# Performance work log

Hardware: AMD Instinct MI355X
Metric: run time of the kernel (lower is better)

The kernel has to match this reference:

```python
import jax, jax.numpy as jnp
import numpy as np

N_QUBITS = 9
N_CIR = 8
CHUNK = 256  # 2**(N_QUBITS-1)
DIM = 512    # 2**N_QUBITS

# Fixed gate sequence (kind, param_index, wires) transcribed from the qnode.
GATES = []
GATES += [("ry", i, (i,)) for i in range(9)]
GATES += [("rx", 9 + i, (i,)) for i in range(9)]
GATES += [("xx", 18 + k, w) for k, w in enumerate([(0,1),(8,7),(1,2),(7,6),(2,3),(6,5),(3,4),(5,4)])]
GATES += [("cry", 26 + k, w) for k, w in enumerate([(0,1),(1,2),(2,3),(8,7),(7,6),(6,5),(5,4),(3,4)])]
GATES += [("ry", 34 + i, (i,)) for i in range(9)]
GATES += [("xy", 43 + k, w) for k, w in enumerate([(4,3),(4,5),(3,2),(5,6),(2,1),(6,7),(1,0),(7,8)])]
GATES += [("crx", 51 + k, w) for k, w in enumerate([(0,1),(2,3),(5,6),(7,8),(1,2),(6,7)])]
GATES += [("rx", 57 + i, (i,)) for i in range(9)]
GATES += [("xx", 66 + k, w) for k, w in enumerate([(0,1),(8,7),(1,2),(7,6),(2,3),(6,5),(3,4),(5,4)])]
GATES += [("cry", 74 + k, w) for k, w in enumerate([(0,1),(1,2),(2,3),(8,7),(7,6),(6,5),(5,4),(3,4)])]
GATES += [("ry", 82 + i, (i,)) for i in range(9)]
GATES += [("xy", 91 + k, w) for k, w in enumerate([(4,3),(4,5),(3,2),(5,6),(2,1),(6,7),(1,0),(7,8)])]
GATES += [("crx", 99 + k, w) for k, w in enumerate([(0,1),(2,3),(5,6),(7,8),(1,2),(6,7)])]
GATES += [("rx", 105 + i, (i,)) for i in range(9)]
assert len(GATES) == 114

C64 = jnp.complex64

def _ry(t):
    c = jnp.cos(t / 2).astype(C64); s = jnp.sin(t / 2).astype(C64)
    return jnp.stack([jnp.stack([c, -s]), jnp.stack([s, c])])

def _rx(t):
    c = jnp.cos(t / 2).astype(C64); s = (-1j * jnp.sin(t / 2)).astype(C64)
    return jnp.stack([jnp.stack([c, s]), jnp.stack([s, c])])

def _xx(t):  # exp(-i t/2 XX)
    c = jnp.cos(t / 2).astype(C64); s = (-1j * jnp.sin(t / 2)).astype(C64)
    z = jnp.zeros_like(c)
    return jnp.stack([jnp.stack([c, z, z, s]), jnp.stack([z, c, s, z]),
                      jnp.stack([z, s, c, z]), jnp.stack([s, z, z, c])])

def _xy(t):  # PennyLane IsingXY
    c = jnp.cos(t / 2).astype(C64); s = (1j * jnp.sin(t / 2)).astype(C64)
    o = jnp.ones_like(c); z = jnp.zeros_like(c)
    return jnp.stack([jnp.stack([o, z, z, z]), jnp.stack([z, c, s, z]),
                      jnp.stack([z, s, c, z]), jnp.stack([z, z, z, o])])

def _ctrl(u2):  # block-diag(I2, u2): control on wires[0], target wires[1]
    z2 = jnp.zeros((2, 2), u2.dtype); i2 = jnp.eye(2, dtype=u2.dtype)
    return jnp.concatenate([jnp.concatenate([i2, z2], 1), jnp.concatenate([z2, u2], 1)], 0)

def _apply1(st, u, w):
    ax = 1 + w
    t = jnp.moveaxis(st, ax, -1)
    t = jnp.einsum('...a,ba->...b', t, u)
    return jnp.moveaxis(t, -1, ax)

def _apply2(st, u, w0, w1):
    a0, a1 = 1 + w0, 1 + w1
    t = jnp.moveaxis(st, (a0, a1), (-2, -1))
    sh = t.shape
    t = jnp.einsum('...a,ba->...b', t.reshape(sh[:-2] + (4,)), u).reshape(sh)
    return jnp.moveaxis(t, (-2, -1), (a0, a1))

def _circuit_probs(feats, qw):
    # feats: (N, 256) float32 -> analytic probs (N, 512)
    f = feats / jnp.linalg.norm(feats, axis=-1, keepdims=True)
    N = f.shape[0]
    # AmplitudeEmbedding on wires [0,1,2,3,5,6,7,8]; wire 4 stays |0>.
    st = jnp.stack([f.reshape(N, 16, 16), jnp.zeros((N, 16, 16), f.dtype)], axis=2)
    st = st.reshape((N,) + (2,) * N_QUBITS).astype(C64)
    for kind, idx, w in GATES:
        t = qw[idx]
        if kind == 'ry':
            st = _apply1(st, _ry(t), w[0])
        elif kind == 'rx':
            st = _apply1(st, _rx(t), w[0])
        elif kind == 'xx':
            st = _apply2(st, _xx(t), *w)
        elif kind == 'xy':
            st = _apply2(st, _xy(t), *w)
        elif kind == 'cry':
            st = _apply2(st, _ctrl(_ry(t)), *w)
        else:  # crx
            st = _apply2(st, _ctrl(_rx(t)), *w)
    return (st.real ** 2 + st.imag ** 2).reshape(N, DIM).astype(jnp.float32)


def setup_inputs() -> dict:
    key = jax.random.key(0)
    k1, k2 = jax.random.split(key)
    B = 4096
    return {
        "input_features": jax.random.normal(k1, (B, N_CIR * CHUNK), dtype=jnp.float32),
        "q_params": jax.random.normal(k2, (114,), dtype=jnp.float32),  # q_delta=1
    }


def reference(input_features, q_params):
    B = input_features.shape[0]
    q_in = jnp.tanh(input_features) * (np.pi / 2.0)
    chunks = q_in.reshape(B * N_CIR, CHUNK)          # per-sample split into 8 chunks of 256
    probs = _circuit_probs(chunks, q_params)          # (B*8, 512), all circuits batched
    return probs.reshape(B, 1024, 2, 2)
```

## Files before the change

kernel.cpp:

```cpp
#include <hip/hip_runtime.h>
#include <utility>

typedef __attribute__((ext_vector_type(8))) short short8;
typedef __attribute__((ext_vector_type(4))) float f32x4;
typedef unsigned short u16;

#define NROW 32768
#define KDIM 256
#define NOUT 512

static constexpr unsigned char cGK[114] = {
  0,0,0,0,0,0,0,0,0,
  1,1,1,1,1,1,1,1,1,
  2,2,2,2,2,2,2,2,
  4,4,4,4,4,4,4,4,
  0,0,0,0,0,0,0,0,0,
  3,3,3,3,3,3,3,3,
  5,5,5,5,5,5,
  1,1,1,1,1,1,1,1,1,
  2,2,2,2,2,2,2,2,
  4,4,4,4,4,4,4,4,
  0,0,0,0,0,0,0,0,0,
  3,3,3,3,3,3,3,3,
  5,5,5,5,5,5,
  1,1,1,1,1,1,1,1,1
};
static constexpr unsigned char cGW0[114] = {
  0,1,2,3,4,5,6,7,8,
  0,1,2,3,4,5,6,7,8,
  0,8,1,7,2,6,3,5,
  0,1,2,8,7,6,5,3,
  0,1,2,3,4,5,6,7,8,
  4,4,3,5,2,6,1,7,
  0,2,5,7,1,6,
  0,1,2,3,4,5,6,7,8,
  0,8,1,7,2,6,3,5,
  0,1,2,8,7,6,5,3,
  0,1,2,3,4,5,6,7,8,
  4,4,3,5,2,6,1,7,
  0,2,5,7,1,6,
  0,1,2,3,4,5,6,7,8
};
static constexpr unsigned char cGW1[114] = {
  0,0,0,0,0,0,0,0,0,
  0,0,0,0,0,0,0,0,0,
  1,7,2,6,3,5,4,4,
  1,2,3,7,6,5,4,4,
  0,0,0,0,0,0,0,0,0,
  3,5,2,6,1,7,0,8,
  1,3,6,8,2,7,
  0,0,0,0,0,0,0,0,0,
  1,7,2,6,3,5,4,4,
  1,2,3,7,6,5,4,4,
  0,0,0,0,0,0,0,0,0,
  3,5,2,6,1,7,0,8,
  1,3,6,8,2,7,
  0,0,0,0,0,0,0,0,0
};

__device__ __forceinline__ u16 f2bf(float f) {
  unsigned int u = __float_as_uint(f);
  u = (u + 0x7fffu + ((u >> 16) & 1u)) >> 16;
  return (u16)u;
}
__device__ __forceinline__ float bf2f(u16 b) {
  return __uint_as_float(((unsigned int)b) << 16);
}

__device__ __forceinline__ float fast_tanh(float x) {
  float xc = fminf(x, 15.f);
  float e = __expf(2.f * xc);
  return 1.f - 2.f * __builtin_amdgcn_rcpf(e + 1.f);
}

typedef const __attribute__((address_space(1))) unsigned int* gptr_t;
typedef __attribute__((address_space(3))) unsigned int* lptr_t;
__device__ __forceinline__ void gload16(const void* g, void* l) {
  __builtin_amdgcn_global_load_lds((gptr_t)g, (lptr_t)l, 16, 0, 0);
}

template <int G>
__device__ __forceinline__ void apply_gate(float (&re)[8], float (&im)[8],
                                           float c0v, float s0v, float c1v,
                                           float s1v, int l) {
  constexpr int kind = cGK[G];
  constexpr int p0 = 8 - cGW0[G];
  constexpr int p1 = 8 - cGW1[G];
  constexpr int m = (kind <= 1) ? (1 << p0)
                  : (kind <= 3) ? ((1 << p0) | (1 << p1))
                  : (1 << p1);
  constexpr int ml = m & 63;
  constexpr int mr = m >> 6;
  float c = __shfl((G < 64) ? c0v : c1v, G & 63, 64);
  float s = __shfl((G < 64) ? s0v : s1v, G & 63, 64);
  float br[8], bi[8];
  #pragma unroll
  for (int r = 0; r < 8; ++r) { br[r] = re[r ^ mr]; bi[r] = im[r ^ mr]; }
  if constexpr (ml != 0) {
    #pragma unroll
    for (int r = 0; r < 8; ++r) {
      br[r] = __shfl_xor(br[r], ml, 64);
      bi[r] = __shfl_xor(bi[r], ml, 64);
    }
  }
  #pragma unroll
  for (int r = 0; r < 8; ++r) {
    const int idx = (r << 6) | l;
    float nre, nim;
    if constexpr (kind == 0) {
      float sg = ((idx >> p0) & 1) ? s : -s;
      nre = c * re[r] + sg * br[r];
      nim = c * im[r] + sg * bi[r];
    } else if constexpr (kind == 1 || kind == 2) {
      nre = c * re[r] + s * bi[r];
      nim = c * im[r] - s * br[r];
    } else if constexpr (kind == 3) {
      bool ap = (((idx >> p0) ^ (idx >> p1)) & 1) != 0;
      nre = ap ? (c * re[r] - s * bi[r]) : re[r];
      nim = ap ? (c * im[r] + s * br[r]) : im[r];
    } else if constexpr (kind == 4) {
      bool ap = ((idx >> p0) & 1) != 0;
      float sg = ((idx >> p1) & 1) ? s : -s;
      nre = ap ? (c * re[r] + sg * br[r]) : re[r];
      nim = ap ? (c * im[r] + sg * bi[r]) : im[r];
    } else {
      bool ap = ((idx >> p0) & 1) != 0;
      nre = ap ? (c * re[r] + s * bi[r]) : re[r];
      nim = ap ? (c * im[r] - s * br[r]) : im[r];
    }
    re[r] = nre; im[r] = nim;
  }
}

template <int... Gs>
__device__ __forceinline__ void apply_all(std::integer_sequence<int, Gs...>,
                                          float (&re)[8], float (&im)[8],
                                          float c0v, float s0v, float c1v,
                                          float s1v, int l) {
  (apply_gate<Gs>(re, im, c0v, s0v, c1v, s1v, l), ...);
}

__global__ void __launch_bounds__(256) prep_build(
    const float* __restrict__ x, const float* __restrict__ qp,
    u16* __restrict__ G, float* __restrict__ invn2, u16* __restrict__ BreT,
    u16* __restrict__ BimT) {
  int bid = blockIdx.x;
  int tid = threadIdx.x;
  int l = tid & 63;
  if (bid < 64) {
    int k = bid * 4 + (tid >> 6);
    float a0 = qp[l] * 0.5f;
    float a1 = (l < 50) ? qp[l + 64] * 0.5f : 0.f;
    float c0v = cosf(a0), s0v = sinf(a0);
    float c1v = cosf(a1), s1v = sinf(a1);

    int col = ((k >> 4) << 5) | (k & 15);
    float re[8], im[8];
    #pragma unroll
    for (int r = 0; r < 8; ++r) {
      re[r] = (r == (col >> 6) && l == (col & 63)) ? 1.f : 0.f;
      im[r] = 0.f;
    }
    apply_all(std::make_integer_sequence<int, 114>{}, re, im, c0v, s0v, c1v,
              s1v, l);
    #pragma unroll
    for (int r = 0; r < 8; ++r) {
      int j = (r << 6) | l;
      BreT[(size_t)j * KDIM + k] = f2bf(re[r]);
      BimT[(size_t)j * KDIM + k] = f2bf(im[r]);
    }
  } else {
    int gid = (bid - 64) * 256 + tid;
    int row = gid >> 6;
    const float H = 1.5707963267948966f;
    float4 v = *(const float4*)(x + ((size_t)row << 8) + l * 4);
    float g0 = fast_tanh(v.x) * H, g1 = fast_tanh(v.y) * H;
    float g2 = fast_tanh(v.z) * H, g3 = fast_tanh(v.w) * H;
    u16 b0 = f2bf(g0), b1 = f2bf(g1), b2 = f2bf(g2), b3 = f2bf(g3);
    float r0 = bf2f(b0), r1 = bf2f(b1), r2 = bf2f(b2), r3 = bf2f(b3);
    float sum = r0 * r0 + r1 * r1 + r2 * r2 + r3 * r3;
    #pragma unroll
    for (int o = 32; o; o >>= 1) sum += __shfl_xor(sum, o, 64);
    ushort4 pk; pk.x = b0; pk.y = b1; pk.z = b2; pk.w = b3;
    *(ushort4*)(G + ((size_t)row << 8) + l * 4) = pk;
    if (l == 0) invn2[row] = 1.0f / sum;
  }
}

__global__ void __launch_bounds__(256) gemm_probs(
    const u16* __restrict__ G, const u16* __restrict__ BreT,
    const u16* __restrict__ BimT, const float* __restrict__ invn2,
    float* __restrict__ out) {
  __shared__ __align__(16) char lds[32768];
  char* sA = lds;
  char* sBre = lds + 16384;
  char* sBim = lds + 24576;
  int tid = threadIdx.x;
  int l = tid & 63;
  int w = tid >> 6;
  int bid = blockIdx.x;
  int nw = (bid & 7) * 256 + (bid >> 3);
  int row0 = (nw >> 3) * 128;
  int n0 = (nw & 7) * 64;

  f32x4 accre[2][4] = {};
  f32x4 accim[2][4] = {};

  for (int k0 = 0; k0 < KDIM; k0 += 64) {
    __syncthreads();
    #pragma unroll
    for (int i = 0; i < 4; ++i) {
      int sg = w * 4 + i;
      int row = sg * 8 + (l >> 3);
      int chunk = (l & 7) ^ (row & 7);
      gload16(G + (size_t)(row0 + row) * KDIM + k0 + chunk * 8, sA + sg * 1024);
    }
    #pragma unroll
    for (int i = 0; i < 2; ++i) {
      int sg = w * 2 + i;
      int rn = sg * 8 + (l >> 3);
      int chunk = (l & 7) ^ (rn & 7);
      size_t off = (size_t)(n0 + rn) * KDIM + k0 + chunk * 8;
      gload16(BreT + off, sBre + sg * 1024);
      gload16(BimT + off, sBim + sg * 1024);
    }
    asm volatile("s_waitcnt vmcnt(0)" ::: "memory");
    __syncthreads();

    #pragma unroll
    for (int kk = 0; kk < 2; ++kk) {
      short8 aF[2], brF[4], biF[4];
      #pragma unroll
      for (int mr = 0; mr < 2; ++mr) {
        int row = w * 32 + mr * 16 + (l & 15);
        int chunk = (kk * 4 + (l >> 4)) ^ (row & 7);
        aF[mr] = *(const short8*)(sA + row * 128 + chunk * 16);
      }
      #pragma unroll
      for (int nb = 0; nb < 4; ++nb) {
        int rn = nb * 16 + (l & 15);
        int chunk = (kk * 4 + (l >> 4)) ^ (rn & 7);
        brF[nb] = *(const short8*)(sBre + rn * 128 + chunk * 16);
        biF[nb] = *(const short8*)(sBim + rn * 128 + chunk * 16);
      }
      #pragma unroll
      for (int mr = 0; mr < 2; ++mr)
        #pragma unroll
        for (int nb = 0; nb < 4; ++nb) {
          accre[mr][nb] = __builtin_amdgcn_mfma_f32_16x16x32_bf16(
              aF[mr], brF[nb], accre[mr][nb], 0, 0, 0);
          accim[mr][nb] = __builtin_amdgcn_mfma_f32_16x16x32_bf16(
              aF[mr], biF[nb], accim[mr][nb], 0, 0, 0);
        }
    }
  }

  #pragma unroll
  for (int mr = 0; mr < 2; ++mr) {
    int rbase = row0 + w * 32 + mr * 16 + (l >> 4) * 4;
    #pragma unroll
    for (int reg = 0; reg < 4; ++reg) {
      float inv = invn2[rbase + reg];
      #pragma unroll
      for (int nb = 0; nb < 4; ++nb) {
        float re = accre[mr][nb][reg];
        float im = accim[mr][nb][reg];
        __builtin_nontemporal_store(
            (re * re + im * im) * inv,
            out + (size_t)(rbase + reg) * NOUT + n0 + nb * 16 + (l & 15));
      }
    }
  }
}

extern "C" void kernel_launch(void* const* d_in, const int* in_sizes, int n_in,
                              void* d_out, int out_size, void* d_ws,
                              size_t ws_size, hipStream_t stream) {
  const float* x = (const float*)d_in[0];
  const float* qp = (const float*)d_in[1];
  float* out = (float*)d_out;
  char* ws = (char*)d_ws;
  u16* G = (u16*)ws;
  u16* BreT = (u16*)(ws + (16u << 20));
  u16* BimT = (u16*)(ws + (16u << 20) + (256u << 10));
  float* invn2 = (float*)(ws + (16u << 20) + (512u << 10));

  hipLaunchKernelGGL(prep_build, dim3(64 + NROW / 4), dim3(256), 0, stream, x,
                     qp, G, invn2, BreT, BimT);
  hipLaunchKernelGGL(gemm_probs, dim3(2048), dim3(256), 0, stream, G, BreT,
                     BimT, invn2, out);
}
```

Measured before the change: 54.56 us.

## Fuse input tanh/bf16 conversion and row norm into GEMM kernel

```diff
diff --git a/kernel.cpp b/kernel.cpp
--- a/kernel.cpp
+++ b/kernel.cpp
@@ -140,61 +140,42 @@
   (apply_gate<Gs>(re, im, c0v, s0v, c1v, s1v, l), ...);
 }
 
-__global__ void __launch_bounds__(256) prep_build(
-    const float* __restrict__ x, const float* __restrict__ qp,
-    u16* __restrict__ G, float* __restrict__ invn2, u16* __restrict__ BreT,
-    u16* __restrict__ BimT) {
-  int bid = blockIdx.x;
+__global__ void __launch_bounds__(256) build_b(const float* __restrict__ qp,
+                                               u16* __restrict__ BreT,
+                                               u16* __restrict__ BimT) {
   int tid = threadIdx.x;
   int l = tid & 63;
-  if (bid < 64) {
-    int k = bid * 4 + (tid >> 6);
-    float a0 = qp[l] * 0.5f;
-    float a1 = (l < 50) ? qp[l + 64] * 0.5f : 0.f;
-    float c0v = cosf(a0), s0v = sinf(a0);
-    float c1v = cosf(a1), s1v = sinf(a1);
-
-    int col = ((k >> 4) << 5) | (k & 15);
-    float re[8], im[8];
-    #pragma unroll
-    for (int r = 0; r < 8; ++r) {
-      re[r] = (r == (col >> 6) && l == (col & 63)) ? 1.f : 0.f;
-      im[r] = 0.f;
-    }
-    apply_all(std::make_integer_sequence<int, 114>{}, re, im, c0v, s0v, c1v,
-              s1v, l);
-    #pragma unroll
-    for (int r = 0; r < 8; ++r) {
-      int j = (r << 6) | l;
-      BreT[(size_t)j * KDIM + k] = f2bf(re[r]);
-      BimT[(size_t)j * KDIM + k] = f2bf(im[r]);
-    }
-  } else {
-    int gid = (bid - 64) * 256 + tid;
-    int row = gid >> 6;
-    const float H = 1.5707963267948966f;
-    float4 v = *(const float4*)(x + ((size_t)row << 8) + l * 4);
-    float g0 = fast_tanh(v.x) * H, g1 = fast_tanh(v.y) * H;
-    float g2 = fast_tanh(v.z) * H, g3 = fast_tanh(v.w) * H;
-    u16 b0 = f2bf(g0), b1 = f2bf(g1), b2 = f2bf(g2), b3 = f2bf(g3);
-    float r0 = bf2f(b0), r1 = bf2f(b1), r2 = bf2f(b2), r3 = bf2f(b3);
-    float sum = r0 * r0 + r1 * r1 + r2 * r2 + r3 * r3;
-    #pragma unroll
-    for (int o = 32; o; o >>= 1) sum += __shfl_xor(sum, o, 64);
-    ushort4 pk; pk.x = b0; pk.y = b1; pk.z = b2; pk.w = b3;
-    *(ushort4*)(G + ((size_t)row << 8) + l * 4) = pk;
-    if (l == 0) invn2[row] = 1.0f / sum;
-  }
-}
-
-__global__ void __launch_bounds__(256) gemm_probs(
-    const u16* __restrict__ G, const u16* __restrict__ BreT,
-    const u16* __restrict__ BimT, const float* __restrict__ invn2,
-    float* __restrict__ out) {
-  __shared__ __align__(16) char lds[32768];
+  int k = blockIdx.x * 4 + (tid >> 6);
+  float a0 = qp[l] * 0.5f;
+  float a1 = (l < 50) ? qp[l + 64] * 0.5f : 0.f;
+  float c0v = cosf(a0), s0v = sinf(a0);
+  float c1v = cosf(a1), s1v = sinf(a1);
+
+  int col = ((k >> 4) << 5) | (k & 15);
+  float re[8], im[8];
+  #pragma unroll
+  for (int r = 0; r < 8; ++r) {
+    re[r] = (r == (col >> 6) && l == (col & 63)) ? 1.f : 0.f;
+    im[r] = 0.f;
+  }
+  apply_all(std::make_integer_sequence<int, 114>{}, re, im, c0v, s0v, c1v,
+            s1v, l);
+  #pragma unroll
+  for (int r = 0; r < 8; ++r) {
+    int j = (r << 6) | l;
+    BreT[(size_t)j * KDIM + k] = f2bf(re[r]);
+    BimT[(size_t)j * KDIM + k] = f2bf(im[r]);
+  }
+}
+
+__global__ void __launch_bounds__(256) gemm_fused(
+    const float* __restrict__ x, const u16* __restrict__ BreT,
+    const u16* __restrict__ BimT, float* __restrict__ out) {
+  __shared__ __align__(16) char lds[33280];
   char* sA = lds;
   char* sBre = lds + 16384;
   char* sBim = lds + 24576;
+  float* rowsum = (float*)(lds + 32768);
   int tid = threadIdx.x;
   int l = tid & 63;
   int w = tid >> 6;
@@ -202,19 +183,17 @@
   int nw = (bid & 7) * 256 + (bid >> 3);
   int row0 = (nw >> 3) * 128;
   int n0 = (nw & 7) * 64;
+  int h = l & 1;
+  int grow = w * 32 + (l >> 1);
+  const float H = 1.5707963267948966f;
 
   f32x4 accre[2][4] = {};
   f32x4 accim[2][4] = {};
-
-  for (int k0 = 0; k0 < KDIM; k0 += 64) {
+  float sumsq = 0.f;
+
+  for (int t = 0; t < 4; ++t) {
+    const int k0 = t * 64;
     __syncthreads();
-    #pragma unroll
-    for (int i = 0; i < 4; ++i) {
-      int sg = w * 4 + i;
-      int row = sg * 8 + (l >> 3);
-      int chunk = (l & 7) ^ (row & 7);
-      gload16(G + (size_t)(row0 + row) * KDIM + k0 + chunk * 8, sA + sg * 1024);
-    }
     #pragma unroll
     for (int i = 0; i < 2; ++i) {
       int sg = w * 2 + i;
@@ -223,6 +202,30 @@
       size_t off = (size_t)(n0 + rn) * KDIM + k0 + chunk * 8;
       gload16(BreT + off, sBre + sg * 1024);
       gload16(BimT + off, sBim + sg * 1024);
+    }
+    const float* xp = x + (size_t)(row0 + grow) * KDIM + k0 + h * 32;
+    float4 v[8];
+    #pragma unroll
+    for (int j = 0; j < 8; ++j) v[j] = *(const float4*)(xp + j * 4);
+    #pragma unroll
+    for (int q = 0; q < 4; ++q) {
+      u16 b[8];
+      #pragma unroll
+      for (int e = 0; e < 4; ++e) {
+        float g0 = fast_tanh(((const float*)&v[2 * q])[e]) * H;
+        float g1 = fast_tanh(((const float*)&v[2 * q + 1])[e]) * H;
+        b[e] = f2bf(g0);
+        b[4 + e] = f2bf(g1);
+      }
+      short8 pk;
+      #pragma unroll
+      for (int e = 0; e < 8; ++e) {
+        float rr = bf2f(b[e]);
+        sumsq += rr * rr;
+        pk[e] = (short)b[e];
+      }
+      int chunk = (h * 4 + q) ^ (grow & 7);
+      *(short8*)(sA + grow * 128 + chunk * 16) = pk;
     }
     asm volatile("s_waitcnt vmcnt(0)" ::: "memory");
     __syncthreads();
@@ -255,19 +258,23 @@
     }
   }
 
+  sumsq += __shfl_xor(sumsq, 1, 64);
+  if (h == 0) rowsum[grow] = sumsq;
+  __syncthreads();
+
   #pragma unroll
   for (int mr = 0; mr < 2; ++mr) {
-    int rbase = row0 + w * 32 + mr * 16 + (l >> 4) * 4;
+    int lrow = w * 32 + mr * 16 + (l >> 4) * 4;
     #pragma unroll
     for (int reg = 0; reg < 4; ++reg) {
-      float inv = invn2[rbase + reg];
+      float inv = 1.0f / rowsum[lrow + reg];
       #pragma unroll
       for (int nb = 0; nb < 4; ++nb) {
         float re = accre[mr][nb][reg];
         float im = accim[mr][nb][reg];
         __builtin_nontemporal_store(
             (re * re + im * im) * inv,
-            out + (size_t)(rbase + reg) * NOUT + n0 + nb * 16 + (l & 15));
+            out + (size_t)(row0 + lrow + reg) * NOUT + n0 + nb * 16 + (l & 15));
       }
     }
   }
@@ -280,13 +287,10 @@
   const float* qp = (const float*)d_in[1];
   float* out = (float*)d_out;
   char* ws = (char*)d_ws;
-  u16* G = (u16*)ws;
-  u16* BreT = (u16*)(ws + (16u << 20));
-  u16* BimT = (u16*)(ws + (16u << 20) + (256u << 10));
-  float* invn2 = (float*)(ws + (16u << 20) + (512u << 10));
-
-  hipLaunchKernelGGL(prep_build, dim3(64 + NROW / 4), dim3(256), 0, stream, x,
-                     qp, G, invn2, BreT, BimT);
-  hipLaunchKernelGGL(gemm_probs, dim3(2048), dim3(256), 0, stream, G, BreT,
-                     BimT, invn2, out);
-}
+  u16* BreT = (u16*)ws;
+  u16* BimT = (u16*)(ws + (256u << 10));
+
+  hipLaunchKernelGGL(build_b, dim3(64), dim3(256), 0, stream, qp, BreT, BimT);
+  hipLaunchKernelGGL(gemm_fused, dim3(2048), dim3(256), 0, stream, x, BreT,
+                     BimT, out);
+}
```

Result: slower. 86.34 us (+58.3%).
